# Kernel tuning notes

Hardware: AMD Instinct MI355X
Metric: run time of the kernel (lower is better)

The kernel has to match this reference:

```python
import jax, jax.numpy as jnp
import numpy as np

T, B, I, H = 256, 128, 256, 1024
G = 4 * H  # LSTM gate size
PI_MIX, SIGMA1, SIGMA2 = 0.75, 1.0, 0.001


def _gauss_logpdf(x, mu, sigma):
    z = (x - mu) / sigma
    return -0.5 * z * z - jnp.log(sigma) - 0.5 * jnp.log(2.0 * jnp.pi)


def _compute_kl(x, mu, sigma):
    log_post = jnp.sum(_gauss_logpdf(x, mu, sigma))
    mix1 = jnp.sum(_gauss_logpdf(x, 0.0, SIGMA1)) + jnp.log(PI_MIX)
    mix2 = jnp.sum(_gauss_logpdf(x, 0.0, SIGMA2)) + jnp.log(1.0 - PI_MIX)
    log_prior = jnp.logaddexp(mix1, mix2)
    return log_post - log_prior


def setup_inputs() -> dict:
    key = jax.random.key(0)
    ks = jax.random.split(key, 13)
    u = lambda k, shape, lo, hi: jax.random.uniform(k, shape, jnp.float32, lo, hi)
    return {
        "x": jax.random.normal(ks[0], (T, B, I), jnp.float32),
        "w_ih_mu": u(ks[1], (G, I), -0.05, 0.05),
        "w_ih_rho": u(ks[2], (G, I), -4.0, -1.0),
        "w_hh_mu": u(ks[3], (G, H), -0.05, 0.05),
        "w_hh_rho": u(ks[4], (G, H), -4.0, -1.0),
        "b_ih_mu": u(ks[5], (G,), -0.05, 0.05),
        "b_ih_rho": u(ks[6], (G,), -4.0, -1.0),
        "b_hh_mu": u(ks[7], (G,), -0.05, 0.05),
        "b_hh_rho": u(ks[8], (G,), -4.0, -1.0),
        "eps_w_ih": jax.random.normal(ks[9], (G, I), jnp.float32),
        "eps_w_hh": jax.random.normal(ks[10], (G, H), jnp.float32),
        "eps_b_ih": jax.random.normal(ks[11], (G,), jnp.float32),
        "eps_b_hh": jax.random.normal(ks[12], (G,), jnp.float32),
    }


def reference(x, w_ih_mu, w_ih_rho, w_hh_mu, w_hh_rho,
              b_ih_mu, b_ih_rho, b_hh_mu, b_hh_rho,
              eps_w_ih, eps_w_hh, eps_b_ih, eps_b_hh):
    # Bayes-by-backprop weight sampling: w = mu + eps * (softplus(rho) + 1e-5)
    s_w_ih = jax.nn.softplus(w_ih_rho) + 1e-5
    s_w_hh = jax.nn.softplus(w_hh_rho) + 1e-5
    s_b_ih = jax.nn.softplus(b_ih_rho) + 1e-5
    s_b_hh = jax.nn.softplus(b_hh_rho) + 1e-5
    w_ih = w_ih_mu + eps_w_ih * s_w_ih  # [4H, I]
    w_hh = w_hh_mu + eps_w_hh * s_w_hh  # [4H, H]
    b_ih = b_ih_mu + eps_b_ih * s_b_ih  # [4H]
    b_hh = b_hh_mu + eps_b_hh * s_b_hh  # [4H]

    kl = (_compute_kl(w_ih, w_ih_mu, s_w_ih)
          + _compute_kl(w_hh, w_hh_mu, s_w_hh)
          + _compute_kl(b_ih, b_ih_mu, s_b_ih)
          + _compute_kl(b_hh, b_hh_mu, s_b_hh))

    # Precompute input projections for all timesteps: [T, B, 4H]
    x_proj = jnp.einsum('tbi,gi->tbg', x, w_ih) + b_ih + b_hh

    h0 = jnp.zeros((B, H), x.dtype)
    c0 = jnp.zeros((B, H), x.dtype)

    def step(carry, xp_t):
        h, c = carry
        gates = xp_t + h @ w_hh.T  # [B, 4H]
        i_g, f_g, g_g, o_g = jnp.split(gates, 4, axis=-1)  # PyTorch gate order i,f,g,o
        c_new = jax.nn.sigmoid(f_g) * c + jax.nn.sigmoid(i_g) * jnp.tanh(g_g)
        h_new = jax.nn.sigmoid(o_g) * jnp.tanh(c_new)
        return (h_new, c_new), h_new

    (h_n, c_n), output = jax.lax.scan(step, (h0, c0), x_proj)
    return output, h_n[None], c_n[None], kl
```

## Files before the change

### kernel.cpp

```cpp
#include <hip/hip_runtime.h>
#include <hip/hip_bf16.h>

typedef unsigned short u16;
typedef __attribute__((ext_vector_type(8))) short short8;
typedef __attribute__((ext_vector_type(4))) float f32x4;

#define T_STEPS 256
#define BATCH   128
#define ISIZE   256
#define HSIZE   1024
#define GSIZE   4096
#define KCAT    1280

#define WCAT_OFF  0UL
#define XBF_OFF   10485760UL
#define ABUF_OFF  27262976UL
#define BCOMB_OFF 27918336UL
#define SUMS_OFF  27934720UL
#define FLAG_OFF  27934848UL
#define XCC_OFF   27935872UL

#define OUT_ELEMS ((size_t)T_STEPS * BATCH * HSIZE)
#define HN_OFF    (OUT_ELEMS)
#define CN_OFF    (OUT_ELEMS + (size_t)BATCH * HSIZE)
#define KL_OFF    (OUT_ELEMS + 2UL * BATCH * HSIZE)

static __device__ __forceinline__ u16 f2bf(float f) {
  union { __hip_bfloat16 h; u16 u; } cv;
  cv.h = __float2bfloat16(f);
  return cv.u;
}

static __device__ __forceinline__ f32x4 mfma16(short8 a, short8 b, f32x4 c) {
  return __builtin_amdgcn_mfma_f32_16x16x32_bf16(a, b, c, 0, 0, 0);
}

static __device__ __forceinline__ float sigm(float v) {
  return 1.0f / (1.0f + __expf(-v));
}
static __device__ __forceinline__ float tanh_(float v) {
  v = fminf(12.0f, fmaxf(-12.0f, v));
  float e = __expf(2.0f * v);
  return (e - 1.0f) / (e + 1.0f);
}

static __device__ void block_reduce_atomic(const float* v, int n, double* dst) {
  __shared__ float red[6][4];
  float loc[6];
  for (int i = 0; i < n; ++i) loc[i] = v[i];
#pragma unroll
  for (int off = 32; off > 0; off >>= 1)
    for (int i = 0; i < n; ++i) loc[i] += __shfl_down(loc[i], off, 64);
  __syncthreads();
  const int wv = threadIdx.x >> 6, ln = threadIdx.x & 63;
  if (ln == 0)
    for (int i = 0; i < n; ++i) red[i][wv] = loc[i];
  __syncthreads();
  if (threadIdx.x == 0)
    for (int i = 0; i < n; ++i)
      atomicAdd(dst + i, (double)(red[i][0] + red[i][1] + red[i][2] + red[i][3]));
  __syncthreads();
}

__global__ __launch_bounds__(256) void prep_kernel(
    const float* __restrict__ x,
    const float* __restrict__ wih_mu, const float* __restrict__ wih_rho,
    const float* __restrict__ whh_mu, const float* __restrict__ whh_rho,
    const float* __restrict__ bih_mu, const float* __restrict__ bih_rho,
    const float* __restrict__ bhh_mu, const float* __restrict__ bhh_rho,
    const float* __restrict__ eih, const float* __restrict__ ehh,
    const float* __restrict__ ebi, const float* __restrict__ ebh,
    u16* __restrict__ wcat, u16* __restrict__ xbf,
    float* __restrict__ bcomb, double* __restrict__ sums)
{
  const unsigned stride = gridDim.x * blockDim.x;
  const unsigned tid0 = blockIdx.x * blockDim.x + threadIdx.x;
  float s[6];

  s[0] = s[1] = s[2] = 0.f;
  for (unsigned i = tid0; i < GSIZE * ISIZE; i += stride) {
    float mu = wih_mu[i], rho = wih_rho[i], ep = eih[i];
    float sg = log1pf(__expf(rho)) + 1e-5f;
    float w  = fmaf(ep, sg, mu);
    unsigned g = i >> 8, k = i & 255u;
    wcat[(size_t)g * KCAT + HSIZE + k] = f2bf(w);
    s[0] += ep * ep; s[1] += __logf(sg); s[2] += w * w;
  }
  block_reduce_atomic(s, 3, sums + 0);

  s[0] = s[1] = s[2] = 0.f;
  for (unsigned i = tid0; i < GSIZE * HSIZE; i += stride) {
    float mu = whh_mu[i], rho = whh_rho[i], ep = ehh[i];
    float sg = log1pf(__expf(rho)) + 1e-5f;
    float w  = fmaf(ep, sg, mu);
    unsigned g = i >> 10, k = i & 1023u;
    wcat[(size_t)g * KCAT + k] = f2bf(w);
    s[0] += ep * ep; s[1] += __logf(sg); s[2] += w * w;
  }
  block_reduce_atomic(s, 3, sums + 3);

  for (int i = 0; i < 6; ++i) s[i] = 0.f;
  for (unsigned i = tid0; i < GSIZE; i += stride) {
    float mu = bih_mu[i], rho = bih_rho[i], ep = ebi[i];
    float sg = log1pf(__expf(rho)) + 1e-5f;
    float w  = fmaf(ep, sg, mu);
    s[0] += ep * ep; s[1] += __logf(sg); s[2] += w * w;
    float mu2 = bhh_mu[i], rho2 = bhh_rho[i], ep2 = ebh[i];
    float sg2 = log1pf(__expf(rho2)) + 1e-5f;
    float w2  = fmaf(ep2, sg2, mu2);
    s[3] += ep2 * ep2; s[4] += __logf(sg2); s[5] += w2 * w2;
    bcomb[i] = w + w2;
  }
  block_reduce_atomic(s, 6, sums + 6);

  for (unsigned i = tid0; i < (unsigned)T_STEPS * BATCH * ISIZE; i += stride)
    xbf[i] = f2bf(x[i]);
}

__global__ void kl_finalize(const double* __restrict__ sums, float* __restrict__ out_kl) {
  const double LOG2PI = 1.8378770664093453;
  const double Ns[4] = {1048576.0, 4194304.0, 4096.0, 4096.0};
  double kl = 0.0;
#pragma unroll
  for (int t = 0; t < 4; ++t) {
    double S1 = sums[t * 3 + 0], S2 = sums[t * 3 + 1], S3 = sums[t * 3 + 2];
    double N = Ns[t];
    double log_post = -0.5 * S1 - S2 - 0.5 * N * LOG2PI;
    double mix1 = -0.5 * S3 - 0.5 * N * LOG2PI + log(0.75);
    double mix2 = -0.5 * S3 * 1.0e6 - N * log(1.0e-3) - 0.5 * N * LOG2PI + log(0.25);
    double mx = fmax(mix1, mix2), mn = fmin(mix1, mix2);
    double log_prior = mx + log1p(exp(mn - mx));
    kl += log_post - log_prior;
  }
  *out_kl = (float)kl;
}

static __device__ __forceinline__ short8 loadA16(const u16* p) {
  short8 r;
  asm volatile("global_load_dwordx4 %0, %1, off sc0" : "=&v"(r) : "v"(p));
  return r;
}

static __device__ __forceinline__ void publish_flag(unsigned* p, unsigned v, bool strong) {
  if (strong)
    __hip_atomic_store(p, v, __ATOMIC_RELEASE, __HIP_MEMORY_SCOPE_AGENT);
  else
    __hip_atomic_store(p, v, __ATOMIC_RELAXED, __HIP_MEMORY_SCOPE_AGENT);
}

static __device__ __forceinline__ void wait_group(const unsigned* f, unsigned target, bool strong) {
  const int lane = threadIdx.x & 63;
  unsigned v;
  do {
    v = (lane < 32) ? __hip_atomic_load(f + lane, __ATOMIC_RELAXED, __HIP_MEMORY_SCOPE_AGENT)
                    : target;
  } while (!__all((int)(v >= target)));
  if (strong)
    __builtin_amdgcn_fence(__ATOMIC_ACQUIRE, "agent");
}

__global__ __launch_bounds__(512, 2) void lstm_kernel(
    const u16* __restrict__ wcat, const u16* __restrict__ xbf,
    u16* __restrict__ abuf, const float* __restrict__ bcomb,
    float* __restrict__ out, unsigned* __restrict__ flags,
    unsigned* __restrict__ xccs)
{
  __shared__ float gates_p[8][16][128];

  const int tid  = threadIdx.x;
  const int wv   = tid >> 6;
  const int lane = tid & 63;
  const int col  = lane & 15;
  const int ksub = lane >> 4;
  const int bm   = blockIdx.x & 7;
  const int bj   = blockIdx.x >> 3;
  const int j0   = bj << 5;
  const int b0   = bm << 4;
  const int wsw  = (ksub & 1) << 4;
  const int sbase = wv * 5;

  unsigned* gflags = flags + bm * 32;

  unsigned xcc;
  asm volatile("s_getreg_b32 %0, hwreg(20, 0, 32)" : "=s"(xcc));
  xcc = (xcc & 15u) + 1u;
  if (tid == 0)
    __hip_atomic_store(xccs + blockIdx.x, xcc, __ATOMIC_RELAXED, __HIP_MEMORY_SCOPE_AGENT);
  bool strong;
  {
    unsigned mine = 0, head = 0;
    int filled;
    do {
      filled = 1;
      if (tid < 256) {
        mine = __hip_atomic_load(xccs + tid, __ATOMIC_RELAXED, __HIP_MEMORY_SCOPE_AGENT);
        head = __hip_atomic_load(xccs + (tid & 7), __ATOMIC_RELAXED, __HIP_MEMORY_SCOPE_AGENT);
        filled = (mine != 0u) && (head != 0u);
      }
    } while (!__syncthreads_and(filled));
    int match = (tid < 256) ? (mine == head) : 1;
    strong = !__syncthreads_and(match);
  }

  short8 wfrag[5][8];
#pragma unroll
  for (int i = 0; i < 5; ++i) {
    const int kk = sbase + i;
#pragma unroll
    for (int n = 0; n < 8; ++n) {
      const int rowg = ((n >> 1) << 10) + j0 + ((n & 1) << 4) + col;
      wfrag[i][n] = *(const short8*)(wcat + (size_t)rowg * KCAT + (kk << 5) + (ksub << 3));
    }
  }
#pragma unroll
  for (int i = 0; i < 5; ++i)
#pragma unroll
    for (int n = 0; n < 8; ++n)
      asm volatile("" : "+v"(wfrag[i][n]));

  const int bl = tid >> 5;
  const int jj = tid & 31;
  const int rsw = ((bl >> 2) & 1) << 4;
  float cbias[4];
#pragma unroll
  for (int g = 0; g < 4; ++g) cbias[g] = bcomb[(g << 10) + j0 + jj];
  float creg = 0.f;

  if (tid == 0) publish_flag(gflags + bj, 1u, strong);

  for (int t = 0; t < T_STEPS; ++t) {
    const u16* curA = abuf + (size_t)(t & 1) * (BATCH * HSIZE);
    u16*       nxtA = abuf + (size_t)((t & 1) ^ 1) * (BATCH * HSIZE);

    short8 av[5];
    const u16* xbase = xbf + ((size_t)t * BATCH + b0 + col) * ISIZE + (ksub << 3);
#pragma unroll
    for (int i = 0; i < 5; ++i) {
      const int kk = sbase + i;
      if (kk >= 32) av[i] = loadA16(xbase + ((kk - 32) << 5));
    }

    if (wv == 0) wait_group(gflags, (unsigned)(t + 1), strong);
    __syncthreads();

    if (!strong) asm volatile("buffer_inv" ::: "memory");

    const u16* hbase = curA + (size_t)(b0 + col) * HSIZE + (ksub << 3);
#pragma unroll
    for (int i = 0; i < 5; ++i) {
      const int kk = sbase + i;
      if (kk < 32) av[i] = loadA16(hbase + (kk << 5));
    }
    asm volatile("s_waitcnt vmcnt(0)" ::: "memory");
    __builtin_amdgcn_sched_barrier(0);

    f32x4 acc[8] = {};
#pragma unroll
    for (int i = 0; i < 5; ++i)
#pragma unroll
      for (int n = 0; n < 8; ++n)
        acc[n] = mfma16(av[i], wfrag[i][n], acc[n]);

#pragma unroll
    for (int n = 0; n < 8; ++n)
#pragma unroll
      for (int v = 0; v < 4; ++v)
        gates_p[wv][ksub * 4 + v][((n << 4) + col) ^ wsw] = acc[n][v];
    __syncthreads();

    float h, cn;
    {
      float gi = 0.f, gf = 0.f, gg = 0.f, go = 0.f;
#pragma unroll
      for (int w = 0; w < 8; ++w) {
        gi += gates_p[w][bl][jj ^ rsw];
        gf += gates_p[w][bl][(32 + jj) ^ rsw];
        gg += gates_p[w][bl][(64 + jj) ^ rsw];
        go += gates_p[w][bl][(96 + jj) ^ rsw];
      }
      gi += cbias[0]; gf += cbias[1]; gg += cbias[2]; go += cbias[3];
      float ig = sigm(gi), fg = sigm(gf), og = sigm(go);
      cn = fg * creg + ig * tanh_(gg);
      creg = cn;
      h = og * tanh_(cn);
      nxtA[(size_t)(b0 + bl) * HSIZE + (j0 + jj)] = f2bf(h);
    }
    __syncthreads();

    if (tid == 0 && t + 1 < T_STEPS)
      publish_flag(gflags + bj, (unsigned)(t + 2), strong);

    {
      size_t hidx = (size_t)(b0 + bl) * HSIZE + (size_t)(j0 + jj);
      out[(size_t)t * (BATCH * HSIZE) + hidx] = h;
      if (t == T_STEPS - 1) {
        out[HN_OFF + hidx] = h;
        out[CN_OFF + hidx] = cn;
      }
    }
  }
}

extern "C" void kernel_launch(void* const* d_in, const int* in_sizes, int n_in,
                              void* d_out, int out_size, void* d_ws, size_t ws_size,
                              hipStream_t stream) {
  (void)in_sizes; (void)n_in; (void)out_size; (void)ws_size;
  const float* x       = (const float*)d_in[0];
  const float* wih_mu  = (const float*)d_in[1];
  const float* wih_rho = (const float*)d_in[2];
  const float* whh_mu  = (const float*)d_in[3];
  const float* whh_rho = (const float*)d_in[4];
  const float* bih_mu  = (const float*)d_in[5];
  const float* bih_rho = (const float*)d_in[6];
  const float* bhh_mu  = (const float*)d_in[7];
  const float* bhh_rho = (const float*)d_in[8];
  const float* eih     = (const float*)d_in[9];
  const float* ehh     = (const float*)d_in[10];
  const float* ebi     = (const float*)d_in[11];
  const float* ebh     = (const float*)d_in[12];

  float* out = (float*)d_out;
  char* ws = (char*)d_ws;
  u16* wcat    = (u16*)(ws + WCAT_OFF);
  u16* xbf     = (u16*)(ws + XBF_OFF);
  u16* abuf    = (u16*)(ws + ABUF_OFF);
  float* bcomb = (float*)(ws + BCOMB_OFF);
  double* sums = (double*)(ws + SUMS_OFF);
  unsigned* flags = (unsigned*)(ws + FLAG_OFF);
  unsigned* xccs  = (unsigned*)(ws + XCC_OFF);

  hipMemsetAsync(ws + SUMS_OFF, 0, 2176, stream);
  hipMemsetAsync(ws + ABUF_OFF, 0, 2UL * BATCH * HSIZE * 2, stream);

  prep_kernel<<<512, 256, 0, stream>>>(x, wih_mu, wih_rho, whh_mu, whh_rho,
      bih_mu, bih_rho, bhh_mu, bhh_rho, eih, ehh, ebi, ebh, wcat, xbf, bcomb, sums);
  kl_finalize<<<1, 1, 0, stream>>>(sums, out + KL_OFF);
  lstm_kernel<<<256, 512, 0, stream>>>(wcat, xbf, abuf, bcomb, out, flags, xccs);
}
```

Before: 0.9995 ms.

## Per-wave fine-grained flag waiting via LDS mirror in relaxed path

In the non-strong (relaxed) path, wave 7, whose K-slices come only from x, computes its MFMA partials immediately, then polls the 32 producer flags and mirrors them into shared memory. The other waves spin on only the flags covering their own K-slices and start loading h and running MFMAs as soon as those producers are ready, removing the block-wide barrier before compute. This is meant to overlap waiting with compute and shorten the per-step critical path. It adds LDS spinning and a goto into the exchange barrier, and it relies on subtle memory-ordering assumptions between the volatile LDS flags and the buffer_inv.

```diff
diff --git a/kernel.cpp b/kernel.cpp
--- a/kernel.cpp
+++ b/kernel.cpp
@@ -148,15 +148,14 @@
     __hip_atomic_store(p, v, __ATOMIC_RELAXED, __HIP_MEMORY_SCOPE_AGENT);
 }
 
-static __device__ __forceinline__ void wait_group(const unsigned* f, unsigned target, bool strong) {
+static __device__ __forceinline__ void wait_group_strong(const unsigned* f, unsigned target) {
   const int lane = threadIdx.x & 63;
   unsigned v;
   do {
     v = (lane < 32) ? __hip_atomic_load(f + lane, __ATOMIC_RELAXED, __HIP_MEMORY_SCOPE_AGENT)
                     : target;
   } while (!__all((int)(v >= target)));
-  if (strong)
-    __builtin_amdgcn_fence(__ATOMIC_ACQUIRE, "agent");
+  __builtin_amdgcn_fence(__ATOMIC_ACQUIRE, "agent");
 }
 
 __global__ __launch_bounds__(512, 2) void lstm_kernel(
@@ -166,6 +165,7 @@
     unsigned* __restrict__ xccs)
 {
   __shared__ float gates_p[8][16][128];
+  __shared__ volatile unsigned fsh[32];
 
   const int tid  = threadIdx.x;
   const int wv   = tid >> 6;
@@ -178,8 +178,11 @@
   const int b0   = bm << 4;
   const int wsw  = (ksub & 1) << 4;
   const int sbase = wv * 5;
+  const int nf = (sbase >= 32) ? 0 : ((32 - sbase) < 5 ? (32 - sbase) : 5);
 
   unsigned* gflags = flags + bm * 32;
+
+  if (tid < 32) fsh[tid] = 0u;
 
   unsigned xcc;
   asm volatile("s_getreg_b32 %0, hwreg(20, 0, 32)" : "=s"(xcc));
@@ -231,6 +234,7 @@
   for (int t = 0; t < T_STEPS; ++t) {
     const u16* curA = abuf + (size_t)(t & 1) * (BATCH * HSIZE);
     u16*       nxtA = abuf + (size_t)((t & 1) ^ 1) * (BATCH * HSIZE);
+    const unsigned target = (unsigned)(t + 1);
 
     short8 av[5];
     const u16* xbase = xbf + ((size_t)t * BATCH + b0 + col) * ISIZE + (ksub << 3);
@@ -240,32 +244,70 @@
       if (kk >= 32) av[i] = loadA16(xbase + ((kk - 32) << 5));
     }
 
-    if (wv == 0) wait_group(gflags, (unsigned)(t + 1), strong);
-    __syncthreads();
+    if (strong) {
+      if (wv == 0) wait_group_strong(gflags, target);
+      __syncthreads();
+    } else if (wv == 7) {
+      asm volatile("s_waitcnt vmcnt(0)" ::: "memory");
+      __builtin_amdgcn_sched_barrier(0);
+      f32x4 acc7[8] = {};
+#pragma unroll
+      for (int i = 0; i < 5; ++i)
+#pragma unroll
+        for (int n = 0; n < 8; ++n)
+          acc7[n] = mfma16(av[i], wfrag[i][n], acc7[n]);
+#pragma unroll
+      for (int n = 0; n < 8; ++n)
+#pragma unroll
+        for (int v = 0; v < 4; ++v)
+          gates_p[7][ksub * 4 + v][((n << 4) + col) ^ wsw] = acc7[n][v];
+      unsigned v;
+      do {
+        v = target;
+        if (lane < 32) {
+          v = __hip_atomic_load(gflags + lane, __ATOMIC_RELAXED, __HIP_MEMORY_SCOPE_AGENT);
+          fsh[lane] = v;
+        }
+      } while (!__all((int)(v >= target)));
+      goto exchange;
+    } else {
+      bool ok;
+      do {
+        ok = true;
+#pragma unroll
+        for (int i = 0; i < 5; ++i)
+          if (i < nf) ok &= (fsh[sbase + i] >= target);
+      } while (!ok);
+    }
 
     if (!strong) asm volatile("buffer_inv" ::: "memory");
-
-    const u16* hbase = curA + (size_t)(b0 + col) * HSIZE + (ksub << 3);
-#pragma unroll
-    for (int i = 0; i < 5; ++i) {
-      const int kk = sbase + i;
-      if (kk < 32) av[i] = loadA16(hbase + (kk << 5));
+    {
+      const u16* hbase = curA + (size_t)(b0 + col) * HSIZE + (ksub << 3);
+#pragma unroll
+      for (int i = 0; i < 5; ++i) {
+        const int kk = sbase + i;
+        if (kk < 32) av[i] = loadA16(hbase + (kk << 5));
+      }
     }
     asm volatile("s_waitcnt vmcnt(0)" ::: "memory");
     __builtin_amdgcn_sched_barrier(0);
 
-    f32x4 acc[8] = {};
-#pragma unroll
-    for (int i = 0; i < 5; ++i)
+    {
+      f32x4 acc[8] = {};
+#pragma unroll
+      for (int i = 0; i < 5; ++i)
+#pragma unroll
+        for (int n = 0; n < 8; ++n)
+          acc[n] = mfma16(av[i], wfrag[i][n], acc[n]);
+
 #pragma unroll
       for (int n = 0; n < 8; ++n)
-        acc[n] = mfma16(av[i], wfrag[i][n], acc[n]);
-
-#pragma unroll
-    for (int n = 0; n < 8; ++n)
-#pragma unroll
-      for (int v = 0; v < 4; ++v)
-        gates_p[wv][ksub * 4 + v][((n << 4) + col) ^ wsw] = acc[n][v];
+#pragma unroll
+        for (int v = 0; v < 4; ++v)
+          gates_p[wv][ksub * 4 + v][((n << 4) + col) ^ wsw] = acc[n][v];
+    }
+
+exchange:
     __syncthreads();
 
     float h, cn;
```

Measured after the change: 1.066 ms. 6.7% more time.
